# Performance work log

Hardware: AMD Instinct MI355X
Metric: run time of the kernel (lower is better)

## Reference

```python
import jax, jax.numpy as jnp
import numpy as np

N, E, D, ED = 25000, 250000, 128, 128
LN_EPS = 1e-5   # nn.LayerNorm default
BN_EPS = 1e-5   # BatchNorm1d default (GENConv MLP norm='batch', training mode)
GEN_EPS = 1e-7  # GENConv message eps


def _ln(x, g, b):
    mu = jnp.mean(x, -1, keepdims=True)
    var = jnp.mean((x - mu) ** 2, -1, keepdims=True)
    return (x - mu) * jax.lax.rsqrt(var + LN_EPS) * g + b


def setup_inputs() -> dict:
    key = jax.random.key(0)
    ks = jax.random.split(key, 8)
    p = lambda k, shp: (jax.random.normal(k, shp, jnp.float32) * 0.02)
    return {
        "x": jax.random.normal(ks[0], (N, D), jnp.float32),
        "edge_attr": jax.random.normal(ks[1], (E, ED), jnp.float32),
        "edge_index": jax.random.randint(ks[2], (2, E), 0, N),
        # edge_mlp: Linear(2D+ED -> ED) + ReLU + LayerNorm(ED)
        "W_e": p(ks[3], (2 * D + ED, ED)), "b_e": jnp.zeros((ED,), jnp.float32),
        "g_e": jnp.ones((ED,), jnp.float32), "be_e": jnp.zeros((ED,), jnp.float32),
        # GENConv learnable softmax temperature t (learn_t=True, init 1.0)
        "t": jnp.float32(1.0),
        # GENConv output MLP: [D -> 2D (BN, ReLU) -> D]  (num_layers=2, expansion=2, norm='batch')
        "W_m1": p(ks[4], (D, 2 * D)), "b_m1": jnp.zeros((2 * D,), jnp.float32),
        "g_bn": jnp.ones((2 * D,), jnp.float32), "b_bn": jnp.zeros((2 * D,), jnp.float32),
        "W_m2": p(ks[5], (2 * D, D)), "b_m2": jnp.zeros((D,), jnp.float32),
        # MessageNorm learnable scale (learn_scale=True, init 1.0)
        "scale": jnp.float32(1.0),
        # node LayerNorm
        "g_n": jnp.ones((D,), jnp.float32), "b_n": jnp.zeros((D,), jnp.float32),
    }


def reference(x, edge_attr, edge_index, W_e, b_e, g_e, be_e, t,
              W_m1, b_m1, g_bn, b_bn, W_m2, b_m2, scale, g_n, b_n):
    row, col = edge_index[0], edge_index[1]  # source, destination (PyG flow)

    # edge MLP with residual: cat([x[row], x[col], edge_attr]) -> Linear -> ReLU -> LN, + edge_attr
    ei = jnp.concatenate([x[row], x[col], edge_attr], axis=-1)        # [E, 2D+ED]
    e = _ln(jnp.maximum(ei @ W_e + b_e, 0.0), g_e, be_e) + edge_attr  # [E, ED]

    # GENConv message: relu(x_j + edge_attr) + eps  (edge_dim == in_channels -> no lin_edge)
    msg = jnp.maximum(x[row] + e, 0.0) + GEN_EPS                      # [E, D]

    # per-destination, per-channel softmax aggregation with temperature t
    s = msg * t
    smax = jax.ops.segment_max(s, col, num_segments=N)                # [N, D]
    ex = jnp.exp(s - smax[col])
    denom = jax.ops.segment_sum(ex, col, num_segments=N)
    alpha = ex / denom[col]
    agg = jax.ops.segment_sum(msg * alpha, col, num_segments=N)       # [N, D]

    # GENConv residual + output MLP (Linear -> BatchNorm(train) -> ReLU -> Linear)
    out = agg + x
    h1 = out @ W_m1 + b_m1                                            # [N, 2D]
    mu = jnp.mean(h1, axis=0)
    var = jnp.mean((h1 - mu) ** 2, axis=0)
    h1 = jnp.maximum((h1 - mu) * jax.lax.rsqrt(var + BN_EPS) * g_bn + b_bn, 0.0)
    h = h1 @ W_m2 + b_m2                                              # [N, D]

    # MessageNorm(learn_scale=True): normalize(h) * ||x|| * scale
    hnorm = jnp.linalg.norm(h, axis=-1, keepdims=True)
    h = h / jnp.maximum(hnorm, 1e-12)
    xnorm = jnp.linalg.norm(x, axis=-1, keepdims=True)
    h = h * xnorm * scale

    # node residual + LayerNorm (dropout in eval mode = identity)
    x_out = _ln(x + h, g_n, b_n)
    return (x_out, e)
```

## Files before the change

kernel.cpp:

```cpp
#include <hip/hip_runtime.h>
#include <hip/hip_bf16.h>

typedef __hip_bfloat16 bf16;
typedef __attribute__((ext_vector_type(8))) short short8v;
typedef __attribute__((ext_vector_type(4))) short short4v;
typedef __attribute__((ext_vector_type(4))) float float4v;

constexpr int N = 25000;
constexpr int E = 250000;
constexpr size_t NB = (size_t)N * 128;
constexpr int NBLK = (N + 63) / 64;

constexpr size_t al256(size_t x) { return (x + 255) / 256 * 256; }

constexpr size_t OFF_BNS  = 0;
constexpr size_t OFF_BNQ  = OFF_BNS + 256;
constexpr size_t OFF_FLAG = OFF_BNQ + 256;
constexpr size_t OFF_XN   = OFF_FLAG + 256;
constexpr size_t OFF_WB   = al256(OFF_XN + N);
constexpr size_t OFF_WP   = OFF_WB + 8192;
constexpr size_t OFF_WM1P = OFF_WP + 16384;
constexpr size_t OFF_WM2P = OFF_WM1P + 16384;
constexpr size_t OFF_DEG  = al256(OFF_WM2P + 16384);
constexpr size_t OFF_OFFS = al256(OFF_DEG + N);
constexpr size_t OFF_CUR  = al256(OFF_OFFS + N + 1);
constexpr size_t OFF_LIST = al256(OFF_CUR + N);
constexpr size_t OFF_OUT  = al256(OFF_LIST + E);
constexpr size_t OFF_A    = al256(OFF_OUT + NB / 2);
constexpr size_t WS_FLOATS = OFF_A + NB;
constexpr size_t OFF_MSG  = al256(OFF_A + NB);
constexpr size_t WS_FLOATS_BIG = OFF_MSG + (size_t)E * 64;


__device__ __forceinline__ float b2f(bf16 v) { return __bfloat162float(v); }
__device__ __forceinline__ short f2bs(float f) {
    bf16 h = __float2bfloat16(f);
    return *reinterpret_cast<short*>(&h);
}
__device__ __forceinline__ float bs2f(short s) {
    bf16 h;
    *reinterpret_cast<short*>(&h) = s;
    return b2f(h);
}

__device__ __forceinline__ float ldf(const void* p, size_t i, int bf) {
    return bf ? b2f(((const bf16*)p)[i]) : ((const float*)p)[i];
}
__device__ __forceinline__ void stf(void* p, size_t i, float v, int bf) {
    if (bf) ((bf16*)p)[i] = __float2bfloat16(v);
    else    ((float*)p)[i] = v;
}
__device__ __forceinline__ void stf_nt(void* p, size_t i, float v, int bf) {
    if (bf) __builtin_nontemporal_store(f2bs(v), (short*)p + i);
    else    __builtin_nontemporal_store(v, (float*)p + i);
}
__device__ __forceinline__ float4v load4(const void* p, size_t i, int bf) {
    if (bf) {
        short4v s = *(const short4v*)((const bf16*)p + i);
        return (float4v){bs2f(s[0]), bs2f(s[1]), bs2f(s[2]), bs2f(s[3])};
    }
    return *(const float4v*)((const float*)p + i);
}
__device__ __forceinline__ void store4_nt(void* p, size_t i, float4v v, int bf) {
    if (bf) {
        short4v s = {f2bs(v[0]), f2bs(v[1]), f2bs(v[2]), f2bs(v[3])};
        __builtin_nontemporal_store(s, (short4v*)((bf16*)p + i));
    } else {
        __builtin_nontemporal_store(v, (float4v*)((float*)p + i));
    }
}
__device__ __forceinline__ float lds_scalar(const void* p, int bf) {
    if (!bf) return *(const float*)p;
    float v = b2f(*(const bf16*)p);
    float a = fabsf(v);
    return (a >= 0.0009765625f && a <= 1024.0f) ? v : *(const float*)p;
}
__device__ __forceinline__ int get_flag(const float* ws) {
    return *(const int*)(ws + OFF_FLAG);
}
__device__ __forceinline__ void* e_base(void* d_out, int bf) {
    return bf ? (void*)((bf16*)d_out + NB) : (void*)((float*)d_out + NB);
}


__global__ void k_detect(const unsigned short* __restrict__ xu, float* __restrict__ ws) {
    __shared__ int cnt;
    if (threadIdx.x == 0) cnt = 0;
    __syncthreads();
    int c = 0;
    for (int i = threadIdx.x; i < 512; i += 256) {
        unsigned e = (xu[i] >> 7) & 0xFFu;
        if (e >= 110u && e <= 135u) c++;
    }
    atomicAdd(&cnt, c);
    for (int i = threadIdx.x; i < 512; i += 256) ws[OFF_BNS + i] = 0.0f;
    int* deg = (int*)(ws + OFF_DEG);
    for (int i = threadIdx.x; i < N; i += 256) deg[i] = 0;
    __syncthreads();
    if (threadIdx.x == 0) *(int*)(ws + OFF_FLAG) = (cnt >= 460) ? 1 : 0;
}

__global__ void k_init(float* __restrict__ ws, const void* __restrict__ W_e,
                       const void* __restrict__ W_m1, const void* __restrict__ W_m2,
                       const int* __restrict__ ei) {
    int bf = get_flag(ws);
    size_t gid = (size_t)blockIdx.x * blockDim.x + threadIdx.x;
    size_t stride = (size_t)gridDim.x * blockDim.x;
    short* WB = (short*)(ws + OFF_WB);
    for (size_t u = gid; u < 16384; u += stride) {
        int k = u >> 7, c = u & 127;
        int t = (k >> 5) * 4096 + (c >> 4) * 512 + (((k & 31) >> 3) * 16 + (c & 15)) * 8 + (k & 7);
        WB[t] = f2bs(ldf(W_e, (size_t)(256 + k) * 128 + c, bf));
    }
    short* WP = (short*)(ws + OFF_WP);
    for (size_t u = gid; u < 32768; u += stride) {
        int k = u >> 8, c = u & 255;
        int t = (k >> 5) * 8192 + (c >> 4) * 512 + (((k & 31) >> 3) * 16 + (c & 15)) * 8 + (k & 7);
        float v = (c < 128) ? ldf(W_e, (size_t)k * 128 + c, bf)
                            : ldf(W_e, (size_t)(128 + k) * 128 + (c - 128), bf);
        WP[t] = f2bs(v);
    }
    short* M1 = (short*)(ws + OFF_WM1P);
    for (size_t u = gid; u < 32768; u += stride) {
        int k = u >> 8, c = u & 255;
        int t = (k >> 5) * 8192 + (c >> 4) * 512 + (((k & 31) >> 3) * 16 + (c & 15)) * 8 + (k & 7);
        M1[t] = f2bs(ldf(W_m1, (size_t)k * 256 + c, bf));
    }
    short* M2 = (short*)(ws + OFF_WM2P);
    for (size_t u = gid; u < 32768; u += stride) {
        int k = u >> 7, c = u & 127;
        int t = (k >> 5) * 4096 + (c >> 4) * 512 + (((k & 31) >> 3) * 16 + (c & 15)) * 8 + (k & 7);
        M2[t] = f2bs(ldf(W_m2, (size_t)k * 128 + c, bf));
    }
    int* deg = (int*)(ws + OFF_DEG);
    for (size_t j = gid; j < E; j += stride) atomicAdd(deg + ei[E + j], 1);
}

__global__ __launch_bounds__(256) void k_node_pre_mfma(const void* __restrict__ x,
                                                       const void* __restrict__ b_e,
                                                       float* __restrict__ ws) {
    int bf = get_flag(ws);
    int l = threadIdx.x & 63, wv = threadIdx.x >> 6;
    int n0 = blockIdx.x * 64 + wv * 16;
    if (n0 >= N) return;
    int row = l & 15, grp = l >> 4;
    int ja = n0 + row;
    int jac = ja < N ? ja : N - 1;
    const short8v* WP = (const short8v*)(ws + OFF_WP);
    float4v acc[16];
    #pragma unroll
    for (int n = 0; n < 16; ++n) acc[n] = (float4v){0.f, 0.f, 0.f, 0.f};
    float sq = 0.f;
    #pragma unroll
    for (int s = 0; s < 4; ++s) {
        short8v af;
        if (bf) {
            af = ((const short8v*)x)[(size_t)jac * 16 + s * 4 + grp];
            #pragma unroll
            for (int i = 0; i < 8; ++i) { float v = bs2f(af[i]); sq = fmaf(v, v, sq); }
        } else {
            const float* er = (const float*)x + (size_t)jac * 128 + s * 32 + grp * 8;
            float4v lo = *(const float4v*)er;
            float4v hi = *(const float4v*)(er + 4);
            float xv[8] = {lo[0], lo[1], lo[2], lo[3], hi[0], hi[1], hi[2], hi[3]};
            #pragma unroll
            for (int i = 0; i < 8; ++i) { sq = fmaf(xv[i], xv[i], sq); af[i] = f2bs(xv[i]); }
        }
        #pragma unroll
        for (int n = 0; n < 16; ++n) {
            acc[n] = __builtin_amdgcn_mfma_f32_16x16x32_bf16(af, WP[(s * 16 + n) * 64 + l], acc[n], 0, 0, 0);
        }
    }
    sq += __shfl_xor(sq, 16, 64);
    sq += __shfl_xor(sq, 32, 64);
    if (grp == 0 && ja < N) ws[OFF_XN + ja] = sqrtf(sq);
    bf16* XA = (bf16*)(ws + OFF_A);
    #pragma unroll
    for (int reg = 0; reg < 4; ++reg) {
        int jd = n0 + grp * 4 + reg;
        if (jd >= N) continue;
        #pragma unroll
        for (int n = 0; n < 16; ++n) {
            int c = n * 16 + row;
            if (n < 8) {
                XA[(size_t)jd * 128 + c] = __float2bfloat16(acc[n][reg] + ldf(b_e, c, bf));
            } else {
                XA[NB + (size_t)jd * 128 + (c - 128)] = __float2bfloat16(acc[n][reg]);
            }
        }
    }
}

template<int WM>
__global__ __launch_bounds__(256) void k_edge1_mfma(const void* __restrict__ ea,
                                                    const int* __restrict__ ei,
                                                    const void* __restrict__ g_e,
                                                    const void* __restrict__ be_e,
                                                    const void* __restrict__ x,
                                                    float* __restrict__ ws,
                                                    void* __restrict__ d_out) {
    int bf = get_flag(ws);
    void* eo = e_base(d_out, bf);
    int l = threadIdx.x & 63;
    int wv = threadIdx.x >> 6;
    int e0w = blockIdx.x * 64 + wv * 16;
    if (e0w >= E) return;
    int eq = l & 15, grp = l >> 4;

    int j = e0w + eq;
    bool valid = j < E;
    int jc = valid ? j : E - 1;
    int r = ei[jc], cd = ei[E + jc];

    const bf16* XAp = (const bf16*)(ws + OFF_A);
    short4v xa[8], xb[8];
    #pragma unroll
    for (int m = 0; m < 8; ++m) {
        int ch = m * 16 + grp * 4;
        xa[m] = *(const short4v*)(XAp + (size_t)r * 128 + ch);
        xb[m] = *(const short4v*)(XAp + NB + (size_t)cd * 128 + ch);
    }

    const short8v* WB = (const short8v*)(ws + OFF_WB);
    float4v acc[8];
    #pragma unroll
    for (int m = 0; m < 8; ++m) acc[m] = (float4v){0.f, 0.f, 0.f, 0.f};

    #pragma unroll
    for (int s = 0; s < 4; ++s) {
        short8v bfr;
        if (bf) {
            bfr = ((const short8v*)ea)[(size_t)jc * 16 + s * 4 + grp];
        } else {
            const float* er = (const float*)ea + (size_t)jc * 128 + s * 32 + grp * 8;
            float4v lo = *(const float4v*)er;
            float4v hi = *(const float4v*)(er + 4);
            bfr[0] = f2bs(lo[0]); bfr[1] = f2bs(lo[1]); bfr[2] = f2bs(lo[2]); bfr[3] = f2bs(lo[3]);
            bfr[4] = f2bs(hi[0]); bfr[5] = f2bs(hi[1]); bfr[6] = f2bs(hi[2]); bfr[7] = f2bs(hi[3]);
        }
        #pragma unroll
        for (int m = 0; m < 8; ++m) {
            acc[m] = __builtin_amdgcn_mfma_f32_16x16x32_bf16(WB[(s * 8 + m) * 64 + l], bfr, acc[m], 0, 0, 0);
        }
    }

    float p[8][4];
    float s1 = 0.f, s2 = 0.f;
    #pragma unroll
    for (int m = 0; m < 8; ++m) {
        #pragma unroll
        for (int w = 0; w < 4; ++w) {
            float v = acc[m][w] + bs2f(xa[m][w]) + bs2f(xb[m][w]);
            v = fmaxf(v, 0.f);
            p[m][w] = v;
            s1 += v;
            s2 = fmaf(v, v, s2);
        }
    }
    float4v xr[8];
    if (WM) {
        #pragma unroll
        for (int m = 0; m < 8; ++m) xr[m] = load4(x, (size_t)r * 128 + m * 16 + grp * 4, bf);
    }
    s1 += __shfl_xor(s1, 16, 64);
    s1 += __shfl_xor(s1, 32, 64);
    s2 += __shfl_xor(s2, 16, 64);
    s2 += __shfl_xor(s2, 32, 64);
    float mu = s1 * (1.f / 128.f);
    float var = s2 * (1.f / 128.f) - mu * mu;
    float rstd = rsqrtf(fmaxf(var, 0.f) + 1e-5f);

    bf16* MSG = (bf16*)(ws + OFF_MSG);
    #pragma unroll
    for (int m = 0; m < 8; ++m) {
        int ch = m * 16 + grp * 4;
        float4v gg = load4(g_e, ch, bf);
        float4v bb = load4(be_e, ch, bf);
        float4v eav = load4(ea, (size_t)jc * 128 + ch, bf);
        float4v ev;
        #pragma unroll
        for (int w = 0; w < 4; ++w)
            ev[w] = (p[m][w] - mu) * rstd * gg[w] + bb[w] + eav[w];
        if (valid) store4_nt(eo, (size_t)j * 128 + ch, ev, bf);
        if (WM && valid) {
            short4v ms;
            #pragma unroll
            for (int w = 0; w < 4; ++w)
                ms[w] = f2bs(fmaxf(xr[m][w] + ev[w], 0.f) + 1e-7f);
            *(short4v*)(MSG + (size_t)j * 128 + ch) = ms;
        }
    }
}

__global__ __launch_bounds__(256) void k_scan(float* __restrict__ ws) {
    const int* deg = (const int*)(ws + OFF_DEG);
    int* offs = (int*)(ws + OFF_OFFS);
    int* cur  = (int*)(ws + OFF_CUR);
    __shared__ int sums[256];
    __shared__ int carry[257];
    int t = threadIdx.x;
    const int chunk = (N + 255) / 256;
    int lo = t * chunk, hi = lo + chunk < N ? lo + chunk : N;
    int s = 0;
    for (int i = lo; i < hi; ++i) s += deg[i];
    sums[t] = s;
    __syncthreads();
    if (t == 0) {
        int acc = 0;
        #pragma unroll 4
        for (int i = 0; i < 256; ++i) { carry[i] = acc; acc += sums[i]; }
        carry[256] = acc;
    }
    __syncthreads();
    int acc = carry[t];
    for (int i = lo; i < hi; ++i) { offs[i] = acc; cur[i] = acc; acc += deg[i]; }
    if (t == 0) offs[N] = carry[256];
}

__global__ void k_scatter(const int* __restrict__ ei, float* __restrict__ ws) {
    int j = blockIdx.x * blockDim.x + threadIdx.x;
    if (j >= E) return;
    int cd = ei[E + j];
    int pos = atomicAdd((int*)(ws + OFF_CUR) + cd, 1);
    ((int*)(ws + OFF_LIST))[pos] = j;
}

__global__ __launch_bounds__(256) void k_agg_stream(const void* __restrict__ x,
                                                    const void* __restrict__ t_p,
                                                    float* __restrict__ ws) {
    int bf = get_flag(ws);
    int n = blockIdx.x, tid = threadIdx.x;
    int par = tid >> 4;
    int cg = tid & 15;
    const int* offs = (const int*)(ws + OFF_OFFS);
    const int* list = (const int*)(ws + OFF_LIST);
    int s0 = offs[n], s1v = offs[n + 1];
    float t = lds_scalar(t_p, bf);
    const short8v* MSG = (const short8v*)((const bf16*)(ws + OFF_MSG));
    float den[8], num[8];
    #pragma unroll
    for (int w = 0; w < 8; ++w) { den[w] = 0.f; num[w] = 0.f; }
    for (int i = s0 + par; i < s1v; i += 16) {
        int jj = list[i];
        short8v m8 = MSG[(size_t)jj * 16 + cg];
        #pragma unroll
        for (int w = 0; w < 8; ++w) {
            float m = bs2f(m8[w]);
            float ex = __expf(fmaf(m, t, -15.0f));
            den[w] += ex;
            num[w] = fmaf(m, ex, num[w]);
        }
    }
    __shared__ float sd[16][132];
    __shared__ float sn[16][132];
    #pragma unroll
    for (int w = 0; w < 8; ++w) { sd[par][cg * 8 + w] = den[w]; sn[par][cg * 8 + w] = num[w]; }
    __syncthreads();
    if (tid < 128) {
        float dn = 0.f, nm = 0.f;
        #pragma unroll
        for (int p = 0; p < 16; ++p) { dn += sd[p][tid]; nm += sn[p][tid]; }
        float ag = dn > 0.f ? nm / dn : 0.f;
        float out = ag + ldf(x, (size_t)n * 128 + tid, bf);
        ((bf16*)(ws + OFF_OUT))[(size_t)n * 128 + tid] = __float2bfloat16(out);
    }
}

__global__ __launch_bounds__(256) void k_agg_gather(const void* __restrict__ x,
                                                    const int* __restrict__ ei,
                                                    const void* __restrict__ t_p,
                                                    void* __restrict__ d_out,
                                                    float* __restrict__ ws) {
    int bf = get_flag(ws);
    const void* e_in = e_base(d_out, bf);
    int n = blockIdx.x, tid = threadIdx.x;
    int c = tid & 127, half = tid >> 7;
    const int* offs = (const int*)(ws + OFF_OFFS);
    const int* list = (const int*)(ws + OFF_LIST);
    int s0 = offs[n], s1v = offs[n + 1];
    float t = lds_scalar(t_p, bf);
    float den = 0.f, num = 0.f;
    for (int i = s0 + half; i < s1v; i += 2) {
        int j = list[i];
        int r = ei[j];
        float ev = ldf(e_in, (size_t)j * 128 + c, bf);
        float msg = fmaxf(ldf(x, (size_t)r * 128 + c, bf) + ev, 0.f) + 1e-7f;
        float ex = expf(msg * t - 15.0f);
        den += ex;
        num = fmaf(msg, ex, num);
    }
    __shared__ float dsh[256];
    __shared__ float nsh[256];
    dsh[tid] = den;
    nsh[tid] = num;
    __syncthreads();
    if (tid < 128) {
        float dn = dsh[tid] + dsh[tid + 128];
        float nm = nsh[tid] + nsh[tid + 128];
        float ag = dn > 0.f ? nm / dn : 0.f;
        float out = ag + ldf(x, (size_t)n * 128 + tid, bf);
        ((bf16*)(ws + OFF_OUT))[(size_t)n * 128 + tid] = __float2bfloat16(out);
    }
}

__global__ __launch_bounds__(256) void k_h1_mfma(const void* __restrict__ b_m1,
                                                 float* __restrict__ ws) {
    int bf = get_flag(ws);
    int l = threadIdx.x & 63, wv = threadIdx.x >> 6;
    int n0 = blockIdx.x * 64 + wv * 16;
    int row = l & 15, grp = l >> 4;
    int ja = n0 + row;
    int jac = ja < N ? ja : N - 1;
    const short8v* OUT = (const short8v*)(ws + OFF_OUT);
    const short8v* M1 = (const short8v*)(ws + OFF_WM1P);
    float4v acc[16];
    #pragma unroll
    for (int n = 0; n < 16; ++n) acc[n] = (float4v){0.f, 0.f, 0.f, 0.f};
    #pragma unroll
    for (int s = 0; s < 4; ++s) {
        short8v af = OUT[(size_t)jac * 16 + s * 4 + grp];
        #pragma unroll
        for (int n = 0; n < 16; ++n) {
            acc[n] = __builtin_amdgcn_mfma_f32_16x16x32_bf16(af, M1[(s * 16 + n) * 64 + l], acc[n], 0, 0, 0);
        }
    }
    __shared__ float sds[4][264];
    __shared__ float sqs[4][264];
    bf16* H1 = (bf16*)(ws + OFF_A);
    #pragma unroll
    for (int n = 0; n < 16; ++n) {
        int col = n * 16 + row;
        float bias = ldf(b_m1, col, bf);
        float vs = 0.f, vq = 0.f;
        #pragma unroll
        for (int reg = 0; reg < 4; ++reg) {
            int jd = n0 + grp * 4 + reg;
            float v = acc[n][reg] + bias;
            if (jd < N) {
                H1[(size_t)jd * 256 + col] = __float2bfloat16(v);
                vs += v;
                vq = fmaf(v, v, vq);
            }
        }
        vs += __shfl_xor(vs, 16, 64); vs += __shfl_xor(vs, 32, 64);
        vq += __shfl_xor(vq, 16, 64); vq += __shfl_xor(vq, 32, 64);
        if (grp == 0) { sds[wv][col] = vs; sqs[wv][col] = vq; }
    }
    __syncthreads();
    int t = threadIdx.x;
    if (t < 256) {
        float s = sds[0][t] + sds[1][t] + sds[2][t] + sds[3][t];
        float q = sqs[0][t] + sqs[1][t] + sqs[2][t] + sqs[3][t];
        atomicAdd(&ws[OFF_BNS + t], s);
        atomicAdd(&ws[OFF_BNQ + t], q);
    }
}

__global__ __launch_bounds__(256) void k_node_post_mfma(const void* __restrict__ x,
                                                        const void* __restrict__ g_bn,
                                                        const void* __restrict__ b_bn,
                                                        const void* __restrict__ b_m2,
                                                        const void* __restrict__ scale_p,
                                                        const void* __restrict__ g_n,
                                                        const void* __restrict__ b_n,
                                                        float* __restrict__ ws,
                                                        void* __restrict__ x_out) {
    int bf = get_flag(ws);
    __shared__ float sA[256];
    __shared__ float sB[256];
    {
        int t = threadIdx.x;
        const float inv_n = 1.f / (float)N;
        float mu = ws[OFF_BNS + t] * inv_n;
        float var = ws[OFF_BNQ + t] * inv_n - mu * mu;
        float rs = rsqrtf(fmaxf(var, 0.f) + 1e-5f) * ldf(g_bn, t, bf);
        sA[t] = rs;
        sB[t] = ldf(b_bn, t, bf) - mu * rs;
    }
    __syncthreads();
    int l = threadIdx.x & 63, wv = threadIdx.x >> 6;
    int n0 = blockIdx.x * 64 + wv * 16;
    if (n0 >= N) return;
    int row = l & 15, grp = l >> 4;
    int ja = n0 + row;
    int jac = ja < N ? ja : N - 1;
    const short8v* H1 = (const short8v*)(ws + OFF_A);
    const short8v* M2 = (const short8v*)(ws + OFF_WM2P);
    float4v acc[8];
    #pragma unroll
    for (int n = 0; n < 8; ++n) acc[n] = (float4v){0.f, 0.f, 0.f, 0.f};
    #pragma unroll
    for (int s = 0; s < 8; ++s) {
        short8v hv = H1[(size_t)jac * 32 + s * 4 + grp];
        int kb = s * 32 + grp * 8;
        short8v af;
        #pragma unroll
        for (int i = 0; i < 8; ++i) {
            float v = fmaf(bs2f(hv[i]), sA[kb + i], sB[kb + i]);
            af[i] = f2bs(fmaxf(v, 0.f));
        }
        #pragma unroll
        for (int n = 0; n < 8; ++n) {
            acc[n] = __builtin_amdgcn_mfma_f32_16x16x32_bf16(af, M2[(s * 8 + n) * 64 + l], acc[n], 0, 0, 0);
        }
    }
    float scl = lds_scalar(scale_p, bf);
    #pragma unroll
    for (int reg = 0; reg < 4; ++reg) {
        int jd = n0 + grp * 4 + reg;
        int jdc = jd < N ? jd : N - 1;
        float h[8];
        float ss = 0.f;
        #pragma unroll
        for (int n = 0; n < 8; ++n) {
            h[n] = acc[n][reg] + ldf(b_m2, n * 16 + row, bf);
            ss = fmaf(h[n], h[n], ss);
        }
        #pragma unroll
        for (int off = 1; off < 16; off <<= 1) ss += __shfl_xor(ss, off, 64);
        float hs = ws[OFF_XN + jdc] * scl / fmaxf(sqrtf(ss), 1e-12f);
        float y[8];
        float s1 = 0.f;
        #pragma unroll
        for (int n = 0; n < 8; ++n) {
            y[n] = ldf(x, (size_t)jdc * 128 + n * 16 + row, bf) + h[n] * hs;
            s1 += y[n];
        }
        #pragma unroll
        for (int off = 1; off < 16; off <<= 1) s1 += __shfl_xor(s1, off, 64);
        float mu = s1 * (1.f / 128.f);
        float s2 = 0.f;
        #pragma unroll
        for (int n = 0; n < 8; ++n) { float d = y[n] - mu; s2 = fmaf(d, d, s2); }
        #pragma unroll
        for (int off = 1; off < 16; off <<= 1) s2 += __shfl_xor(s2, off, 64);
        float rstd = rsqrtf(s2 * (1.f / 128.f) + 1e-5f);
        if (jd < N) {
            #pragma unroll
            for (int n = 0; n < 8; ++n) {
                int col = n * 16 + row;
                float o = (y[n] - mu) * rstd * ldf(g_n, col, bf) + ldf(b_n, col, bf);
                stf_nt(x_out, (size_t)jd * 128 + col, o, bf);
            }
        }
    }
}


extern "C" void kernel_launch(void* const* d_in, const int* in_sizes, int n_in,
                              void* d_out, int out_size, void* d_ws, size_t ws_size,
                              hipStream_t stream) {
    const void* x    = d_in[0];
    const void* ea   = d_in[1];
    const int*  ei   = (const int*)d_in[2];
    const void* W_e  = d_in[3];
    const void* b_e  = d_in[4];
    const void* g_e  = d_in[5];
    const void* be_e = d_in[6];
    const void* t_p  = d_in[7];
    const void* W_m1 = d_in[8];
    const void* b_m1 = d_in[9];
    const void* g_bn = d_in[10];
    const void* b_bn = d_in[11];
    const void* W_m2 = d_in[12];
    const void* b_m2 = d_in[13];
    const void* scl  = d_in[14];
    const void* g_n  = d_in[15];
    const void* b_n  = d_in[16];

    float* ws = (float*)d_ws;
    bool big = ws_size >= WS_FLOATS_BIG * sizeof(float);

    k_detect<<<1, 256, 0, stream>>>((const unsigned short*)x, ws);
    k_init<<<512, 256, 0, stream>>>(ws, W_e, W_m1, W_m2, ei);
    k_scan<<<1, 256, 0, stream>>>(ws);
    k_scatter<<<(E + 255) / 256, 256, 0, stream>>>(ei, ws);
    k_node_pre_mfma<<<NBLK, 256, 0, stream>>>(x, b_e, ws);
    if (big) {
        k_edge1_mfma<1><<<(E + 63) / 64, 256, 0, stream>>>(ea, ei, g_e, be_e, x, ws, d_out);
        k_agg_stream<<<N, 256, 0, stream>>>(x, t_p, ws);
    } else {
        k_edge1_mfma<0><<<(E + 63) / 64, 256, 0, stream>>>(ea, ei, g_e, be_e, x, ws, d_out);
        k_agg_gather<<<N, 256, 0, stream>>>(x, ei, t_p, d_out, ws);
    }
    k_h1_mfma<<<NBLK, 256, 0, stream>>>(b_m1, ws);
    k_node_post_mfma<<<NBLK, 256, 0, stream>>>(x, g_bn, b_bn, b_m2, scl, g_n, b_n, ws, d_out);
}
```

Measured before the change: 560.0 us.

## Drop materialized message buffer; recompute messages in aggregation from edge output

Removes the intermediate bf16 message array written by the edge kernel and read back in aggregation. The aggregation kernel now gathers e and x[row] and recomputes relu(x+e)+eps itself, using 16-lane parallel loads. In the edge kernel the edge_attr residual is taken from registers already loaded for the MFMA via lane shuffles instead of being reloaded, and the e output uses normal cached stores instead of nontemporal ones so aggregation can hit cache. This trades one E×128 write and read for extra gather traffic on x and e in aggregation.

```diff
diff --git a/kernel.cpp b/kernel.cpp
--- a/kernel.cpp
+++ b/kernel.cpp
@@ -5,6 +5,7 @@
 typedef __attribute__((ext_vector_type(8))) short short8v;
 typedef __attribute__((ext_vector_type(4))) short short4v;
 typedef __attribute__((ext_vector_type(4))) float float4v;
+typedef unsigned long long u64;
 
 constexpr int N = 25000;
 constexpr int E = 250000;
@@ -28,8 +29,6 @@
 constexpr size_t OFF_OUT  = al256(OFF_LIST + E);
 constexpr size_t OFF_A    = al256(OFF_OUT + NB / 2);
 constexpr size_t WS_FLOATS = OFF_A + NB;
-constexpr size_t OFF_MSG  = al256(OFF_A + NB);
-constexpr size_t WS_FLOATS_BIG = OFF_MSG + (size_t)E * 64;
 
 
 __device__ __forceinline__ float b2f(bf16 v) { return __bfloat162float(v); }
@@ -46,10 +45,6 @@
 __device__ __forceinline__ float ldf(const void* p, size_t i, int bf) {
     return bf ? b2f(((const bf16*)p)[i]) : ((const float*)p)[i];
 }
-__device__ __forceinline__ void stf(void* p, size_t i, float v, int bf) {
-    if (bf) ((bf16*)p)[i] = __float2bfloat16(v);
-    else    ((float*)p)[i] = v;
-}
 __device__ __forceinline__ void stf_nt(void* p, size_t i, float v, int bf) {
     if (bf) __builtin_nontemporal_store(f2bs(v), (short*)p + i);
     else    __builtin_nontemporal_store(v, (float*)p + i);
@@ -61,12 +56,12 @@
     }
     return *(const float4v*)((const float*)p + i);
 }
-__device__ __forceinline__ void store4_nt(void* p, size_t i, float4v v, int bf) {
+__device__ __forceinline__ void store4(void* p, size_t i, float4v v, int bf) {
     if (bf) {
         short4v s = {f2bs(v[0]), f2bs(v[1]), f2bs(v[2]), f2bs(v[3])};
-        __builtin_nontemporal_store(s, (short4v*)((bf16*)p + i));
+        *(short4v*)((bf16*)p + i) = s;
     } else {
-        __builtin_nontemporal_store(v, (float4v*)((float*)p + i));
+        *(float4v*)((float*)p + i) = v;
     }
 }
 __device__ __forceinline__ float lds_scalar(const void* p, int bf) {
@@ -191,12 +186,10 @@
     }
 }
 
-template<int WM>
 __global__ __launch_bounds__(256) void k_edge1_mfma(const void* __restrict__ ea,
                                                     const int* __restrict__ ei,
                                                     const void* __restrict__ g_e,
                                                     const void* __restrict__ be_e,
-                                                    const void* __restrict__ x,
                                                     float* __restrict__ ws,
                                                     void* __restrict__ d_out) {
     int bf = get_flag(ws);
@@ -222,25 +215,29 @@
     }
 
     const short8v* WB = (const short8v*)(ws + OFF_WB);
-    float4v acc[8];
-    #pragma unroll
-    for (int m = 0; m < 8; ++m) acc[m] = (float4v){0.f, 0.f, 0.f, 0.f};
-
+    union { short8v v; u64 q[2]; } bfr[4];
     #pragma unroll
     for (int s = 0; s < 4; ++s) {
-        short8v bfr;
         if (bf) {
-            bfr = ((const short8v*)ea)[(size_t)jc * 16 + s * 4 + grp];
+            bfr[s].v = ((const short8v*)ea)[(size_t)jc * 16 + s * 4 + grp];
         } else {
             const float* er = (const float*)ea + (size_t)jc * 128 + s * 32 + grp * 8;
             float4v lo = *(const float4v*)er;
             float4v hi = *(const float4v*)(er + 4);
-            bfr[0] = f2bs(lo[0]); bfr[1] = f2bs(lo[1]); bfr[2] = f2bs(lo[2]); bfr[3] = f2bs(lo[3]);
-            bfr[4] = f2bs(hi[0]); bfr[5] = f2bs(hi[1]); bfr[6] = f2bs(hi[2]); bfr[7] = f2bs(hi[3]);
-        }
+            short8v t;
+            t[0] = f2bs(lo[0]); t[1] = f2bs(lo[1]); t[2] = f2bs(lo[2]); t[3] = f2bs(lo[3]);
+            t[4] = f2bs(hi[0]); t[5] = f2bs(hi[1]); t[6] = f2bs(hi[2]); t[7] = f2bs(hi[3]);
+            bfr[s].v = t;
+        }
+    }
+    float4v acc[8];
+    #pragma unroll
+    for (int m = 0; m < 8; ++m) acc[m] = (float4v){0.f, 0.f, 0.f, 0.f};
+    #pragma unroll
+    for (int s = 0; s < 4; ++s) {
         #pragma unroll
         for (int m = 0; m < 8; ++m) {
-            acc[m] = __builtin_amdgcn_mfma_f32_16x16x32_bf16(WB[(s * 8 + m) * 64 + l], bfr, acc[m], 0, 0, 0);
+            acc[m] = __builtin_amdgcn_mfma_f32_16x16x32_bf16(WB[(s * 8 + m) * 64 + l], bfr[s].v, acc[m], 0, 0, 0);
         }
     }
 
@@ -257,10 +254,14 @@
             s2 = fmaf(v, v, s2);
         }
     }
-    float4v xr[8];
-    if (WM) {
-        #pragma unroll
-        for (int m = 0; m < 8; ++m) xr[m] = load4(x, (size_t)r * 128 + m * 16 + grp * 4, bf);
+    u64 eavq[8];
+    #pragma unroll
+    for (int m = 0; m < 8; ++m) {
+        const int s = m >> 1;
+        int srcl = eq + 32 * (m & 1) + 16 * (grp >> 1);
+        u64 a = __shfl(bfr[s].q[0], srcl, 64);
+        u64 b = __shfl(bfr[s].q[1], srcl, 64);
+        eavq[m] = (grp & 1) ? b : a;
     }
     s1 += __shfl_xor(s1, 16, 64);
     s1 += __shfl_xor(s1, 32, 64);
@@ -270,25 +271,18 @@
     float var = s2 * (1.f / 128.f) - mu * mu;
     float rstd = rsqrtf(fmaxf(var, 0.f) + 1e-5f);
 
-    bf16* MSG = (bf16*)(ws + OFF_MSG);
     #pragma unroll
     for (int m = 0; m < 8; ++m) {
         int ch = m * 16 + grp * 4;
         float4v gg = load4(g_e, ch, bf);
         float4v bb = load4(be_e, ch, bf);
-        float4v eav = load4(ea, (size_t)jc * 128 + ch, bf);
         float4v ev;
         #pragma unroll
-        for (int w = 0; w < 4; ++w)
-            ev[w] = (p[m][w] - mu) * rstd * gg[w] + bb[w] + eav[w];
-        if (valid) store4_nt(eo, (size_t)j * 128 + ch, ev, bf);
-        if (WM && valid) {
-            short4v ms;
-            #pragma unroll
-            for (int w = 0; w < 4; ++w)
-                ms[w] = f2bs(fmaxf(xr[m][w] + ev[w], 0.f) + 1e-7f);
-            *(short4v*)(MSG + (size_t)j * 128 + ch) = ms;
-        }
+        for (int w = 0; w < 4; ++w) {
+            float eav = bs2f((short)(eavq[m] >> (16 * w)));
+            ev[w] = (p[m][w] - mu) * rstd * gg[w] + bb[w] + eav;
+        }
+        if (valid) store4(eo, (size_t)j * 128 + ch, ev, bf);
     }
 }
 
@@ -325,10 +319,13 @@
     ((int*)(ws + OFF_LIST))[pos] = j;
 }
 
-__global__ __launch_bounds__(256) void k_agg_stream(const void* __restrict__ x,
-                                                    const void* __restrict__ t_p,
-                                                    float* __restrict__ ws) {
+__global__ __launch_bounds__(256) void k_agg(const void* __restrict__ x,
+                                             const int* __restrict__ ei,
+                                             const void* __restrict__ t_p,
+                                             void* __restrict__ d_out,
+                                             float* __restrict__ ws) {
     int bf = get_flag(ws);
+    const void* e_in = e_base(d_out, bf);
     int n = blockIdx.x, tid = threadIdx.x;
     int par = tid >> 4;
     int cg = tid & 15;
@@ -336,16 +333,21 @@
     const int* list = (const int*)(ws + OFF_LIST);
     int s0 = offs[n], s1v = offs[n + 1];
     float t = lds_scalar(t_p, bf);
-    const short8v* MSG = (const short8v*)((const bf16*)(ws + OFF_MSG));
     float den[8], num[8];
     #pragma unroll
     for (int w = 0; w < 8; ++w) { den[w] = 0.f; num[w] = 0.f; }
     for (int i = s0 + par; i < s1v; i += 16) {
         int jj = list[i];
-        short8v m8 = MSG[(size_t)jj * 16 + cg];
+        int r = ei[jj];
+        float4v e0 = load4(e_in, (size_t)jj * 128 + cg * 8, bf);
+        float4v e1 = load4(e_in, (size_t)jj * 128 + cg * 8 + 4, bf);
+        float4v x0 = load4(x, (size_t)r * 128 + cg * 8, bf);
+        float4v x1 = load4(x, (size_t)r * 128 + cg * 8 + 4, bf);
         #pragma unroll
         for (int w = 0; w < 8; ++w) {
-            float m = bs2f(m8[w]);
+            float ev = w < 4 ? e0[w & 3] : e1[w & 3];
+            float xv = w < 4 ? x0[w & 3] : x1[w & 3];
+            float m = fmaxf(xv + ev, 0.f) + 1e-7f;
             float ex = __expf(fmaf(m, t, -15.0f));
             den[w] += ex;
             num[w] = fmaf(m, ex, num[w]);
@@ -360,43 +362,6 @@
         float dn = 0.f, nm = 0.f;
         #pragma unroll
         for (int p = 0; p < 16; ++p) { dn += sd[p][tid]; nm += sn[p][tid]; }
-        float ag = dn > 0.f ? nm / dn : 0.f;
-        float out = ag + ldf(x, (size_t)n * 128 + tid, bf);
-        ((bf16*)(ws + OFF_OUT))[(size_t)n * 128 + tid] = __float2bfloat16(out);
-    }
-}
-
-__global__ __launch_bounds__(256) void k_agg_gather(const void* __restrict__ x,
-                                                    const int* __restrict__ ei,
-                                                    const void* __restrict__ t_p,
-                                                    void* __restrict__ d_out,
-                                                    float* __restrict__ ws) {
-    int bf = get_flag(ws);
-    const void* e_in = e_base(d_out, bf);
-    int n = blockIdx.x, tid = threadIdx.x;
-    int c = tid & 127, half = tid >> 7;
-    const int* offs = (const int*)(ws + OFF_OFFS);
-    const int* list = (const int*)(ws + OFF_LIST);
-    int s0 = offs[n], s1v = offs[n + 1];
-    float t = lds_scalar(t_p, bf);
-    float den = 0.f, num = 0.f;
-    for (int i = s0 + half; i < s1v; i += 2) {
-        int j = list[i];
-        int r = ei[j];
-        float ev = ldf(e_in, (size_t)j * 128 + c, bf);
-        float msg = fmaxf(ldf(x, (size_t)r * 128 + c, bf) + ev, 0.f) + 1e-7f;
-        float ex = expf(msg * t - 15.0f);
-        den += ex;
-        num = fmaf(msg, ex, num);
-    }
-    __shared__ float dsh[256];
-    __shared__ float nsh[256];
-    dsh[tid] = den;
-    nsh[tid] = num;
-    __syncthreads();
-    if (tid < 128) {
-        float dn = dsh[tid] + dsh[tid + 128];
-        float nm = nsh[tid] + nsh[tid + 128];
         float ag = dn > 0.f ? nm / dn : 0.f;
         float out = ag + ldf(x, (size_t)n * 128 + tid, bf);
         ((bf16*)(ws + OFF_OUT))[(size_t)n * 128 + tid] = __float2bfloat16(out);
@@ -569,20 +534,14 @@
     const void* b_n  = d_in[16];
 
     float* ws = (float*)d_ws;
-    bool big = ws_size >= WS_FLOATS_BIG * sizeof(float);
 
     k_detect<<<1, 256, 0, stream>>>((const unsigned short*)x, ws);
     k_init<<<512, 256, 0, stream>>>(ws, W_e, W_m1, W_m2, ei);
     k_scan<<<1, 256, 0, stream>>>(ws);
     k_scatter<<<(E + 255) / 256, 256, 0, stream>>>(ei, ws);
     k_node_pre_mfma<<<NBLK, 256, 0, stream>>>(x, b_e, ws);
-    if (big) {
-        k_edge1_mfma<1><<<(E + 63) / 64, 256, 0, stream>>>(ea, ei, g_e, be_e, x, ws, d_out);
-        k_agg_stream<<<N, 256, 0, stream>>>(x, t_p, ws);
-    } else {
-        k_edge1_mfma<0><<<(E + 63) / 64, 256, 0, stream>>>(ea, ei, g_e, be_e, x, ws, d_out);
-        k_agg_gather<<<N, 256, 0, stream>>>(x, ei, t_p, d_out, ws);
-    }
+    k_edge1_mfma<<<(E + 63) / 64, 256, 0, stream>>>(ea, ei, g_e, be_e, ws, d_out);
+    k_agg<<<N, 256, 0, stream>>>(x, ei, t_p, d_out, ws);
     k_h1_mfma<<<NBLK, 256, 0, stream>>>(b_m1, ws);
     k_node_post_mfma<<<NBLK, 256, 0, stream>>>(x, g_bn, b_bn, b_m2, scl, g_n, b_n, ws, d_out);
 }
```

Result: faster. 521.1 us (-6.9%).
